# Kernel optimization log

Measured on AMD Instinct MI355X. Metric: run time of the kernel, lower is better.

Reference implementation:

```python
import jax, jax.numpy as jnp
import numpy as np

N_NODES = 100000
N_EDGES = 3200000
R0, R1, R2, N1 = 16, 8, 16, 32


def setup_inputs() -> dict:
    key = jax.random.key(0)
    ks = jax.random.split(key, 12)
    x = jax.random.normal(ks[0], (N_NODES, R0), dtype=jnp.float32)
    edge_index = jax.random.randint(ks[1], (2, N_EDGES), 0, N_NODES, dtype=jnp.int64)
    s = 0.1
    return {
        "x": x,
        "edge_index": edge_index,
        # GraphConv 1: lin_rel (weight+bias) applied to aggregated neighbors, lin_root (no bias) to self
        "W_rel1": jax.random.normal(ks[2], (R0, R1), dtype=jnp.float32) * s,
        "b_rel1": jnp.zeros((R1,), dtype=jnp.float32),
        "W_root1": jax.random.normal(ks[3], (R0, R1), dtype=jnp.float32) * s,
        # GraphConv 2
        "W_rel2": jax.random.normal(ks[4], (R1, R2), dtype=jnp.float32) * s,
        "b_rel2": jnp.zeros((R2,), dtype=jnp.float32),
        "W_root2": jax.random.normal(ks[5], (R1, R2), dtype=jnp.float32) * s,
        # fc layers
        "W_fc1": jax.random.normal(ks[6], (R2, N1), dtype=jnp.float32) * s,
        "b_fc1": jnp.zeros((N1,), dtype=jnp.float32),
        "W_fc2": jax.random.normal(ks[7], (N1, 1), dtype=jnp.float32) * s,
        "b_fc2": jnp.zeros((1,), dtype=jnp.float32),
    }


def _graph_conv(x, src, dst, W_rel, b_rel, W_root):
    # GraphConv with aggr='add': out_i = lin_rel(sum_{j->i} x_j) + lin_root(x_i)
    agg = jax.ops.segment_sum(x[src], dst, num_segments=N_NODES)  # [N, d_in]
    return agg @ W_rel + b_rel + x @ W_root


def reference(x, edge_index,
              W_rel1, b_rel1, W_root1,
              W_rel2, b_rel2, W_root2,
              W_fc1, b_fc1, W_fc2, b_fc2):
    src, dst = edge_index[0], edge_index[1]
    h = jax.nn.relu(_graph_conv(x, src, dst, W_rel1, b_rel1, W_root1))
    h = jax.nn.relu(_graph_conv(h, src, dst, W_rel2, b_rel2, W_root2))
    h = jax.nn.relu(h @ W_fc1 + b_fc1)
    out = h @ W_fc2 + b_fc2  # [N, 1]
    return out - jnp.mean(out)
```

## Files before the change

kernel.cpp:

```cpp
#include <hip/hip_runtime.h>

#define NN 100000
#define NE 3200000
#define BSH 7
#define BNODES 128
#define NBUCK 782
#define BCAP 4800
#define BIN_CHUNK 8192
#define NBIN_BLOCKS ((NE + BIN_CHUNK - 1) / BIN_CHUNK)

#define S1 2097152.0f
#define S2 524288.0f
#define INV_S1 (1.0f / S1)
#define INV_S2 (1.0f / S2)

__global__ void node_layer1(const float* __restrict__ x,
                            const float* __restrict__ Wrel1,
                            const float* __restrict__ brel1,
                            const float* __restrict__ Wroot1,
                            int* __restrict__ y1q,
                            int* __restrict__ initq,
                            int* __restrict__ bucketCnt ) {
    __shared__ float sW[16 * 8];
    __shared__ float sR[16 * 8];
    __shared__ float sb[8];
    int t = threadIdx.x;
    if (t < 128) { sW[t] = Wrel1[t]; sR[t] = Wroot1[t]; }
    if (t < 8)   { sb[t] = brel1[t]; }
    if (blockIdx.x == 0) {
        for (int k = t; k < NBUCK + 1; k += 256) bucketCnt[k] = 0;
    }
    __syncthreads();

    int i = blockIdx.x * blockDim.x + t;
    if (i >= NN) return;

    const float4* xp = (const float4*)(x + (size_t)i * 16);
    float4 x0 = xp[0], x1 = xp[1], x2 = xp[2], x3 = xp[3];
    float xi[16] = {x0.x, x0.y, x0.z, x0.w, x1.x, x1.y, x1.z, x1.w,
                    x2.x, x2.y, x2.z, x2.w, x3.x, x3.y, x3.z, x3.w};

    float y[8], r[8];
#pragma unroll
    for (int j = 0; j < 8; ++j) { y[j] = 0.0f; r[j] = sb[j]; }
#pragma unroll
    for (int k = 0; k < 16; ++k) {
        float xv = xi[k];
#pragma unroll
        for (int j = 0; j < 8; ++j) {
            y[j] = fmaf(xv, sW[k * 8 + j], y[j]);
            r[j] = fmaf(xv, sR[k * 8 + j], r[j]);
        }
    }
    int4* yp = (int4*)(y1q + (size_t)i * 8);
    int4* ap = (int4*)(initq + (size_t)i * 8);
    int4 q0, q1, p0, p1;
    q0.x = __float2int_rn(y[0] * S1); q0.y = __float2int_rn(y[1] * S1);
    q0.z = __float2int_rn(y[2] * S1); q0.w = __float2int_rn(y[3] * S1);
    q1.x = __float2int_rn(y[4] * S1); q1.y = __float2int_rn(y[5] * S1);
    q1.z = __float2int_rn(y[6] * S1); q1.w = __float2int_rn(y[7] * S1);
    p0.x = __float2int_rn(r[0] * S1); p0.y = __float2int_rn(r[1] * S1);
    p0.z = __float2int_rn(r[2] * S1); p0.w = __float2int_rn(r[3] * S1);
    p1.x = __float2int_rn(r[4] * S1); p1.y = __float2int_rn(r[5] * S1);
    p1.z = __float2int_rn(r[6] * S1); p1.w = __float2int_rn(r[7] * S1);
    yp[0] = q0; yp[1] = q1;
    ap[0] = p0; ap[1] = p1;
}

__global__ __launch_bounds__(1024) void binning(const int* __restrict__ src,
                                                const int* __restrict__ dst,
                                                int* __restrict__ bucketCnt,
                                                int* __restrict__ bpay) {
    __shared__ int stage[BIN_CHUNK];
    __shared__ int hist[NBUCK];
    __shared__ int loff[NBUCK + 1];
    __shared__ int gbase[NBUCK];
    __shared__ int psum[1024];

    int t = threadIdx.x;
    int e0 = blockIdx.x * BIN_CHUNK;
    int nE = NE - e0; if (nE > BIN_CHUNK) nE = BIN_CHUNK;
    int nv = nE >> 2;

    if (t < NBUCK) hist[t] = 0;
    __syncthreads();

    const int4* dst4 = (const int4*)(dst + e0);
    const int4* src4 = (const int4*)(src + e0);

    for (int k = t; k < nv; k += 1024) {
        int4 d4 = dst4[k];
        atomicAdd(&hist[d4.x >> BSH], 1);
        atomicAdd(&hist[d4.y >> BSH], 1);
        atomicAdd(&hist[d4.z >> BSH], 1);
        atomicAdd(&hist[d4.w >> BSH], 1);
    }
    __syncthreads();

    int c = (t < NBUCK) ? hist[t] : 0;
    psum[t] = c;
    __syncthreads();
    for (int off = 1; off < 1024; off <<= 1) {
        int u = (t >= off) ? psum[t - off] : 0;
        __syncthreads();
        psum[t] += u;
        __syncthreads();
    }
    if (t < NBUCK) loff[t] = psum[t] - c;
    if (t == 0) loff[NBUCK] = nE;
    __syncthreads();

    if (t < NBUCK) {
        gbase[t] = c ? atomicAdd(&bucketCnt[t], c) : 0;
        hist[t] = loff[t];
    }
    __syncthreads();

    for (int k = t; k < nv; k += 1024) {
        int4 d4 = dst4[k];
        int4 s4 = src4[k];
        int b, r;
        b = d4.x >> BSH; r = atomicAdd(&hist[b], 1);
        stage[r] = ((d4.x & (BNODES - 1)) << 17) | s4.x;
        b = d4.y >> BSH; r = atomicAdd(&hist[b], 1);
        stage[r] = ((d4.y & (BNODES - 1)) << 17) | s4.y;
        b = d4.z >> BSH; r = atomicAdd(&hist[b], 1);
        stage[r] = ((d4.z & (BNODES - 1)) << 17) | s4.z;
        b = d4.w >> BSH; r = atomicAdd(&hist[b], 1);
        stage[r] = ((d4.w & (BNODES - 1)) << 17) | s4.w;
    }
    __syncthreads();

    for (int p = t; p < nE; p += 1024) {
        int lo = 0, hi = NBUCK - 1;
        while (lo < hi) {
            int mid = (lo + hi + 1) >> 1;
            if (loff[mid] <= p) lo = mid; else hi = mid - 1;
        }
        int ob = gbase[lo] + (p - loff[lo]);
        if (ob < BCAP) bpay[lo * BCAP + ob] = stage[p];
    }
}

__global__ __launch_bounds__(512, 6) void bucket_agg1(const int* __restrict__ bucketCnt,
                                                      const int* __restrict__ bpay,
                                                      const int* __restrict__ y1q,
                                                      int* __restrict__ h1q ) {
    __shared__ int qacc[BNODES * 8];
    int t = threadIdx.x;
    int b = blockIdx.x;
    int gb = b * BCAP;
    int fbase = b * (BNODES * 8);

    for (int k = t; k < BNODES * 8; k += 512) {
        int gi = fbase + k;
        qacc[k] = (gi < NN * 8) ? h1q[gi] : 0;
    }
    int C = bucketCnt[b]; if (C > BCAP) C = BCAP;
    __syncthreads();

    int f = t & 7, g = t >> 3;
    const int4* bp4 = (const int4*)(bpay + gb);
    int iters = C >> 9;
    for (int it = 0; it < iters; ++it) {
        int4 va = bp4[(it << 7) + (g << 1)];
        int4 vb = bp4[(it << 7) + (g << 1) + 1];
        int a0 = y1q[((va.x & 0x1FFFF) << 3) + f];
        int a1 = y1q[((va.y & 0x1FFFF) << 3) + f];
        int a2 = y1q[((va.z & 0x1FFFF) << 3) + f];
        int a3 = y1q[((va.w & 0x1FFFF) << 3) + f];
        int a4 = y1q[((vb.x & 0x1FFFF) << 3) + f];
        int a5 = y1q[((vb.y & 0x1FFFF) << 3) + f];
        int a6 = y1q[((vb.z & 0x1FFFF) << 3) + f];
        int a7 = y1q[((vb.w & 0x1FFFF) << 3) + f];
        atomicAdd(&qacc[((va.x >> 17) << 3) + f], a0);
        atomicAdd(&qacc[((va.y >> 17) << 3) + f], a1);
        atomicAdd(&qacc[((va.z >> 17) << 3) + f], a2);
        atomicAdd(&qacc[((va.w >> 17) << 3) + f], a3);
        atomicAdd(&qacc[((vb.x >> 17) << 3) + f], a4);
        atomicAdd(&qacc[((vb.y >> 17) << 3) + f], a5);
        atomicAdd(&qacc[((vb.z >> 17) << 3) + f], a6);
        atomicAdd(&qacc[((vb.w >> 17) << 3) + f], a7);
    }
    for (int e = (iters << 9) + g; e < C; e += 64) {
        int v = bpay[gb + e];
        int a = y1q[((v & 0x1FFFF) << 3) + f];
        atomicAdd(&qacc[((v >> 17) << 3) + f], a);
    }
    __syncthreads();

    for (int k = t; k < BNODES * 8; k += 512) {
        int gi = fbase + k;
        if (gi < NN * 8) {
            float h = (float)qacc[k] * INV_S1;
            h = h > 0.0f ? h : 0.0f;
            h1q[gi] = __float2int_rn(h * S2);
        }
    }
}

__global__ __launch_bounds__(512, 6) void bucket_agg2_tail(const int* __restrict__ bucketCnt,
                                                           const int* __restrict__ bpay,
                                                           const int* __restrict__ h1q,
                                                           const float* __restrict__ Wrel2,
                                                           const float* __restrict__ brel2,
                                                           const float* __restrict__ Wroot2,
                                                           const float* __restrict__ Wfc1,
                                                           const float* __restrict__ bfc1,
                                                           const float* __restrict__ Wfc2,
                                                           const float* __restrict__ bfc2,
                                                           float* __restrict__ out,
                                                           float* __restrict__ gsum) {
    __shared__ int qacc[BNODES * 8];
    __shared__ float sWrel2[128], sWroot2[128], sbrel2[16];
    __shared__ float sWfc1[512], sbfc1[32], sWfc2[32];
    __shared__ float sbfc2;
    __shared__ float wsum[8];

    int t = threadIdx.x;
    int b = blockIdx.x;
    int gb = b * BCAP;
    int n0 = b * BNODES;

    for (int k = t; k < BNODES * 8; k += 512) qacc[k] = 0;
    sWfc1[t] = Wfc1[t];
    if (t < 128) { sWrel2[t] = Wrel2[t]; sWroot2[t] = Wroot2[t]; }
    if (t >= 128 && t < 144) sbrel2[t - 128] = brel2[t - 128];
    if (t >= 192 && t < 224) { sbfc1[t - 192] = bfc1[t - 192]; sWfc2[t - 192] = Wfc2[t - 192]; }
    if (t == 256) sbfc2 = bfc2[0];
    int C = bucketCnt[b]; if (C > BCAP) C = BCAP;
    __syncthreads();

    int f = t & 7, g = t >> 3;
    const int4* bp4 = (const int4*)(bpay + gb);
    int iters = C >> 9;
    for (int it = 0; it < iters; ++it) {
        int4 va = bp4[(it << 7) + (g << 1)];
        int4 vb = bp4[(it << 7) + (g << 1) + 1];
        int a0 = h1q[((va.x & 0x1FFFF) << 3) + f];
        int a1 = h1q[((va.y & 0x1FFFF) << 3) + f];
        int a2 = h1q[((va.z & 0x1FFFF) << 3) + f];
        int a3 = h1q[((va.w & 0x1FFFF) << 3) + f];
        int a4 = h1q[((vb.x & 0x1FFFF) << 3) + f];
        int a5 = h1q[((vb.y & 0x1FFFF) << 3) + f];
        int a6 = h1q[((vb.z & 0x1FFFF) << 3) + f];
        int a7 = h1q[((vb.w & 0x1FFFF) << 3) + f];
        atomicAdd(&qacc[((va.x >> 17) << 3) + f], a0);
        atomicAdd(&qacc[((va.y >> 17) << 3) + f], a1);
        atomicAdd(&qacc[((va.z >> 17) << 3) + f], a2);
        atomicAdd(&qacc[((va.w >> 17) << 3) + f], a3);
        atomicAdd(&qacc[((vb.x >> 17) << 3) + f], a4);
        atomicAdd(&qacc[((vb.y >> 17) << 3) + f], a5);
        atomicAdd(&qacc[((vb.z >> 17) << 3) + f], a6);
        atomicAdd(&qacc[((vb.w >> 17) << 3) + f], a7);
    }
    for (int e = (iters << 9) + g; e < C; e += 64) {
        int v = bpay[gb + e];
        int a = h1q[((v & 0x1FFFF) << 3) + f];
        atomicAdd(&qacc[((v >> 17) << 3) + f], a);
    }
    __syncthreads();

    float o = 0.0f;
    int node = n0 + t;
    if (t < BNODES && node < NN) {
        const int4* hp = (const int4*)(h1q + (size_t)node * 8);
        int4 ha = hp[0], hb = hp[1];
        float h1v[8] = {ha.x * INV_S2, ha.y * INV_S2, ha.z * INV_S2, ha.w * INV_S2,
                        hb.x * INV_S2, hb.y * INV_S2, hb.z * INV_S2, hb.w * INV_S2};
        float s2[8];
#pragma unroll
        for (int j = 0; j < 8; ++j) s2[j] = (float)qacc[t * 8 + j] * INV_S2;

        float h2[16];
#pragma unroll
        for (int j = 0; j < 16; ++j) h2[j] = sbrel2[j];
#pragma unroll
        for (int k = 0; k < 8; ++k) {
            float sv = s2[k], hv = h1v[k];
#pragma unroll
            for (int j = 0; j < 16; ++j) {
                h2[j] = fmaf(sv, sWrel2[k * 16 + j], h2[j]);
                h2[j] = fmaf(hv, sWroot2[k * 16 + j], h2[j]);
            }
        }
#pragma unroll
        for (int j = 0; j < 16; ++j) h2[j] = h2[j] > 0.0f ? h2[j] : 0.0f;

        o = sbfc2;
#pragma unroll
        for (int m = 0; m < 32; ++m) {
            float a = sbfc1[m];
#pragma unroll
            for (int j = 0; j < 16; ++j) a = fmaf(h2[j], sWfc1[j * 32 + m], a);
            a = a > 0.0f ? a : 0.0f;
            o = fmaf(a, sWfc2[m], o);
        }
        out[node] = o;
    }

    float v = o;
#pragma unroll
    for (int off = 32; off > 0; off >>= 1) v += __shfl_down(v, off);
    int lane = t & 63, w = t >> 6;
    if (lane == 0) wsum[w] = v;
    __syncthreads();
    if (t == 0) {
        float s = 0.0f;
#pragma unroll
        for (int k = 0; k < 8; ++k) s += wsum[k];
        atomicAdd(gsum, s);
    }
}

__global__ void subtract_mean(float* __restrict__ out,
                              const float* __restrict__ gsum) {
    int i = blockIdx.x * blockDim.x + threadIdx.x;
    if (i < NN) out[i] -= (*gsum) * (1.0f / (float)NN);
}

extern "C" void kernel_launch(void* const* d_in, const int* in_sizes, int n_in,
                              void* d_out, int out_size, void* d_ws, size_t ws_size,
                              hipStream_t stream) {
    const float* x      = (const float*)d_in[0];
    const int*   ei     = (const int*)d_in[1];
    const float* Wrel1  = (const float*)d_in[2];
    const float* brel1  = (const float*)d_in[3];
    const float* Wroot1 = (const float*)d_in[4];
    const float* Wrel2  = (const float*)d_in[5];
    const float* brel2  = (const float*)d_in[6];
    const float* Wroot2 = (const float*)d_in[7];
    const float* Wfc1   = (const float*)d_in[8];
    const float* bfc1   = (const float*)d_in[9];
    const float* Wfc2   = (const float*)d_in[10];
    const float* bfc2   = (const float*)d_in[11];
    float* out = (float*)d_out;
    float* ws  = (float*)d_ws;

    int*   y1q       = (int*)ws;
    int*   h1q       = (int*)(ws + 800000);
    int*   bucketCnt = (int*)(ws + 1600000);
    float* gsum      = ws + 1600782;
    int*   bpay      = (int*)(ws + 1600783);

    const int* src = ei;
    const int* dst = ei + NE;

    node_layer1<<<(NN + 255) / 256, 256, 0, stream>>>(x, Wrel1, brel1, Wroot1,
                                                      y1q, h1q, bucketCnt);
    binning<<<NBIN_BLOCKS, 1024, 0, stream>>>(src, dst, bucketCnt, bpay);
    bucket_agg1<<<NBUCK, 512, 0, stream>>>(bucketCnt, bpay, y1q, h1q);
    bucket_agg2_tail<<<NBUCK, 512, 0, stream>>>(bucketCnt, bpay, h1q,
                                                Wrel2, brel2, Wroot2,
                                                Wfc1, bfc1, Wfc2, bfc2, out, gsum);
    subtract_mean<<<(NN + 255) / 256, 256, 0, stream>>>(out, gsum);
}
```

Before: 183.1 us.

## Fuse layer-1 node transform into binning kernel and streamline bucket scatter

Merges the node_layer1 kernel into the binning kernel as extra blocks, and zeroes bucket counters with a memset instead of inside a kernel. The binning path keeps each thread's edges in registers instead of reloading them, replaces the shared-memory block scan with wave shuffle scans, and stores each edge's global destination next to its payload so the final scatter needs no binary search. It also raises the occupancy hint on bucket_agg1. The aim is to cut launches, syncs and per-edge search work, at the cost of more shared memory per binning block (int2 staging).

```diff
diff --git a/kernel.cpp b/kernel.cpp
--- a/kernel.cpp
+++ b/kernel.cpp
@@ -8,76 +8,75 @@
 #define BCAP 4800
 #define BIN_CHUNK 8192
 #define NBIN_BLOCKS ((NE + BIN_CHUNK - 1) / BIN_CHUNK)
+#define NL1_BLOCKS ((NN + 1023) / 1024)
 
 #define S1 2097152.0f
 #define S2 524288.0f
 #define INV_S1 (1.0f / S1)
 #define INV_S2 (1.0f / S2)
 
-__global__ void node_layer1(const float* __restrict__ x,
-                            const float* __restrict__ Wrel1,
-                            const float* __restrict__ brel1,
-                            const float* __restrict__ Wroot1,
-                            int* __restrict__ y1q,
-                            int* __restrict__ initq,
-                            int* __restrict__ bucketCnt ) {
-    __shared__ float sW[16 * 8];
-    __shared__ float sR[16 * 8];
-    __shared__ float sb[8];
+__global__ __launch_bounds__(1024, 8) void bin_and_l1(
+        const float* __restrict__ x,
+        const float* __restrict__ Wrel1,
+        const float* __restrict__ brel1,
+        const float* __restrict__ Wroot1,
+        const int* __restrict__ src,
+        const int* __restrict__ dst,
+        int* __restrict__ y1q,
+        int* __restrict__ initq,
+        int* __restrict__ bucketCnt,
+        int* __restrict__ bpay) {
     int t = threadIdx.x;
-    if (t < 128) { sW[t] = Wrel1[t]; sR[t] = Wroot1[t]; }
-    if (t < 8)   { sb[t] = brel1[t]; }
-    if (blockIdx.x == 0) {
-        for (int k = t; k < NBUCK + 1; k += 256) bucketCnt[k] = 0;
-    }
-    __syncthreads();
-
-    int i = blockIdx.x * blockDim.x + t;
-    if (i >= NN) return;
-
-    const float4* xp = (const float4*)(x + (size_t)i * 16);
-    float4 x0 = xp[0], x1 = xp[1], x2 = xp[2], x3 = xp[3];
-    float xi[16] = {x0.x, x0.y, x0.z, x0.w, x1.x, x1.y, x1.z, x1.w,
-                    x2.x, x2.y, x2.z, x2.w, x3.x, x3.y, x3.z, x3.w};
-
-    float y[8], r[8];
-#pragma unroll
-    for (int j = 0; j < 8; ++j) { y[j] = 0.0f; r[j] = sb[j]; }
-#pragma unroll
-    for (int k = 0; k < 16; ++k) {
-        float xv = xi[k];
-#pragma unroll
-        for (int j = 0; j < 8; ++j) {
-            y[j] = fmaf(xv, sW[k * 8 + j], y[j]);
-            r[j] = fmaf(xv, sR[k * 8 + j], r[j]);
-        }
-    }
-    int4* yp = (int4*)(y1q + (size_t)i * 8);
-    int4* ap = (int4*)(initq + (size_t)i * 8);
-    int4 q0, q1, p0, p1;
-    q0.x = __float2int_rn(y[0] * S1); q0.y = __float2int_rn(y[1] * S1);
-    q0.z = __float2int_rn(y[2] * S1); q0.w = __float2int_rn(y[3] * S1);
-    q1.x = __float2int_rn(y[4] * S1); q1.y = __float2int_rn(y[5] * S1);
-    q1.z = __float2int_rn(y[6] * S1); q1.w = __float2int_rn(y[7] * S1);
-    p0.x = __float2int_rn(r[0] * S1); p0.y = __float2int_rn(r[1] * S1);
-    p0.z = __float2int_rn(r[2] * S1); p0.w = __float2int_rn(r[3] * S1);
-    p1.x = __float2int_rn(r[4] * S1); p1.y = __float2int_rn(r[5] * S1);
-    p1.z = __float2int_rn(r[6] * S1); p1.w = __float2int_rn(r[7] * S1);
-    yp[0] = q0; yp[1] = q1;
-    ap[0] = p0; ap[1] = p1;
-}
-
-__global__ __launch_bounds__(1024) void binning(const int* __restrict__ src,
-                                                const int* __restrict__ dst,
-                                                int* __restrict__ bucketCnt,
-                                                int* __restrict__ bpay) {
-    __shared__ int stage[BIN_CHUNK];
-    __shared__ int hist[NBUCK];
-    __shared__ int loff[NBUCK + 1];
-    __shared__ int gbase[NBUCK];
-    __shared__ int psum[1024];
-
-    int t = threadIdx.x;
+
+    if (blockIdx.x >= NBIN_BLOCKS) {
+        __shared__ float sW[16 * 8];
+        __shared__ float sR[16 * 8];
+        __shared__ float sb[8];
+        if (t < 128) { sW[t] = Wrel1[t]; sR[t] = Wroot1[t]; }
+        if (t < 8)   { sb[t] = brel1[t]; }
+        __syncthreads();
+
+        int i = (blockIdx.x - NBIN_BLOCKS) * 1024 + t;
+        if (i >= NN) return;
+
+        const float4* xp = (const float4*)(x + (size_t)i * 16);
+        float4 x0 = xp[0], x1 = xp[1], x2 = xp[2], x3 = xp[3];
+        float xi[16] = {x0.x, x0.y, x0.z, x0.w, x1.x, x1.y, x1.z, x1.w,
+                        x2.x, x2.y, x2.z, x2.w, x3.x, x3.y, x3.z, x3.w};
+
+        float y[8], r[8];
+#pragma unroll
+        for (int j = 0; j < 8; ++j) { y[j] = 0.0f; r[j] = sb[j]; }
+#pragma unroll
+        for (int k = 0; k < 16; ++k) {
+            float xv = xi[k];
+#pragma unroll
+            for (int j = 0; j < 8; ++j) {
+                y[j] = fmaf(xv, sW[k * 8 + j], y[j]);
+                r[j] = fmaf(xv, sR[k * 8 + j], r[j]);
+            }
+        }
+        int4* yp = (int4*)(y1q + (size_t)i * 8);
+        int4* ap = (int4*)(initq + (size_t)i * 8);
+        int4 q0, q1, p0, p1;
+        q0.x = __float2int_rn(y[0] * S1); q0.y = __float2int_rn(y[1] * S1);
+        q0.z = __float2int_rn(y[2] * S1); q0.w = __float2int_rn(y[3] * S1);
+        q1.x = __float2int_rn(y[4] * S1); q1.y = __float2int_rn(y[5] * S1);
+        q1.z = __float2int_rn(y[6] * S1); q1.w = __float2int_rn(y[7] * S1);
+        p0.x = __float2int_rn(r[0] * S1); p0.y = __float2int_rn(r[1] * S1);
+        p0.z = __float2int_rn(r[2] * S1); p0.w = __float2int_rn(r[3] * S1);
+        p1.x = __float2int_rn(r[4] * S1); p1.y = __float2int_rn(r[5] * S1);
+        p1.z = __float2int_rn(r[6] * S1); p1.w = __float2int_rn(r[7] * S1);
+        yp[0] = q0; yp[1] = q1;
+        ap[0] = p0; ap[1] = p1;
+        return;
+    }
+
+    __shared__ int2 stage2[BIN_CHUNK];
+    __shared__ int  hist[NBUCK];
+    __shared__ int  gdelta[NBUCK];
+    __shared__ int  wsum16[16];
+
     int e0 = blockIdx.x * BIN_CHUNK;
     int nE = NE - e0; if (nE > BIN_CHUNK) nE = BIN_CHUNK;
     int nv = nE >> 2;
@@ -88,61 +87,77 @@
     const int4* dst4 = (const int4*)(dst + e0);
     const int4* src4 = (const int4*)(src + e0);
 
-    for (int k = t; k < nv; k += 1024) {
-        int4 d4 = dst4[k];
-        atomicAdd(&hist[d4.x >> BSH], 1);
-        atomicAdd(&hist[d4.y >> BSH], 1);
-        atomicAdd(&hist[d4.z >> BSH], 1);
-        atomicAdd(&hist[d4.w >> BSH], 1);
+    int4 d0_, s0_, d1_, s1_;
+    bool h0 = (t < nv), h1 = (t + 1024 < nv);
+    if (h0) {
+        d0_ = dst4[t]; s0_ = src4[t];
+        atomicAdd(&hist[d0_.x >> BSH], 1);
+        atomicAdd(&hist[d0_.y >> BSH], 1);
+        atomicAdd(&hist[d0_.z >> BSH], 1);
+        atomicAdd(&hist[d0_.w >> BSH], 1);
+    }
+    if (h1) {
+        d1_ = dst4[t + 1024]; s1_ = src4[t + 1024];
+        atomicAdd(&hist[d1_.x >> BSH], 1);
+        atomicAdd(&hist[d1_.y >> BSH], 1);
+        atomicAdd(&hist[d1_.z >> BSH], 1);
+        atomicAdd(&hist[d1_.w >> BSH], 1);
     }
     __syncthreads();
 
     int c = (t < NBUCK) ? hist[t] : 0;
-    psum[t] = c;
-    __syncthreads();
-    for (int off = 1; off < 1024; off <<= 1) {
-        int u = (t >= off) ? psum[t - off] : 0;
-        __syncthreads();
-        psum[t] += u;
-        __syncthreads();
-    }
-    if (t < NBUCK) loff[t] = psum[t] - c;
-    if (t == 0) loff[NBUCK] = nE;
-    __syncthreads();
+    int lane = t & 63, w = t >> 6;
+    int pref = c;
+#pragma unroll
+    for (int off = 1; off < 64; off <<= 1) {
+        int u = __shfl_up(pref, off);
+        if (lane >= off) pref += u;
+    }
+    if (lane == 63) wsum16[w] = pref;
+    __syncthreads();
+    if (t < 16) {
+        int s = wsum16[t];
+#pragma unroll
+        for (int off = 1; off < 16; off <<= 1) {
+            int u = __shfl_up(s, off);
+            if (t >= off) s += u;
+        }
+        wsum16[t] = s;
+    }
+    __syncthreads();
+    int base = w ? wsum16[w - 1] : 0;
+    int excl = base + pref - c;
 
     if (t < NBUCK) {
-        gbase[t] = c ? atomicAdd(&bucketCnt[t], c) : 0;
-        hist[t] = loff[t];
-    }
-    __syncthreads();
-
-    for (int k = t; k < nv; k += 1024) {
-        int4 d4 = dst4[k];
-        int4 s4 = src4[k];
-        int b, r;
-        b = d4.x >> BSH; r = atomicAdd(&hist[b], 1);
-        stage[r] = ((d4.x & (BNODES - 1)) << 17) | s4.x;
-        b = d4.y >> BSH; r = atomicAdd(&hist[b], 1);
-        stage[r] = ((d4.y & (BNODES - 1)) << 17) | s4.y;
-        b = d4.z >> BSH; r = atomicAdd(&hist[b], 1);
-        stage[r] = ((d4.z & (BNODES - 1)) << 17) | s4.z;
-        b = d4.w >> BSH; r = atomicAdd(&hist[b], 1);
-        stage[r] = ((d4.w & (BNODES - 1)) << 17) | s4.w;
-    }
+        int gb0 = c ? atomicAdd(&bucketCnt[t], c) : 0;
+        hist[t] = excl;
+        gdelta[t] = t * BCAP + gb0 - excl;
+    }
+    __syncthreads();
+
+#define PLACE1(dv, sv) do {                                              \
+        int b_ = (dv) >> BSH;                                            \
+        int r_ = atomicAdd(&hist[b_], 1);                                \
+        int ga_ = r_ + gdelta[b_];                                       \
+        int2 e_; e_.x = (((dv) & (BNODES - 1)) << 17) | (sv);            \
+        e_.y = (ga_ < (b_ + 1) * BCAP) ? ga_ : -1;                       \
+        stage2[r_] = e_;                                                 \
+    } while (0)
+
+    if (h0) { PLACE1(d0_.x, s0_.x); PLACE1(d0_.y, s0_.y);
+              PLACE1(d0_.z, s0_.z); PLACE1(d0_.w, s0_.w); }
+    if (h1) { PLACE1(d1_.x, s1_.x); PLACE1(d1_.y, s1_.y);
+              PLACE1(d1_.z, s1_.z); PLACE1(d1_.w, s1_.w); }
+#undef PLACE1
     __syncthreads();
 
     for (int p = t; p < nE; p += 1024) {
-        int lo = 0, hi = NBUCK - 1;
-        while (lo < hi) {
-            int mid = (lo + hi + 1) >> 1;
-            if (loff[mid] <= p) lo = mid; else hi = mid - 1;
-        }
-        int ob = gbase[lo] + (p - loff[lo]);
-        if (ob < BCAP) bpay[lo * BCAP + ob] = stage[p];
-    }
-}
-
-__global__ __launch_bounds__(512, 6) void bucket_agg1(const int* __restrict__ bucketCnt,
+        int2 e = stage2[p];
+        if (e.y >= 0) bpay[e.y] = e.x;
+    }
+}
+
+__global__ __launch_bounds__(512, 8) void bucket_agg1(const int* __restrict__ bucketCnt,
                                                       const int* __restrict__ bpay,
                                                       const int* __restrict__ y1q,
                                                       int* __restrict__ h1q ) {
@@ -346,9 +361,10 @@
     const int* src = ei;
     const int* dst = ei + NE;
 
-    node_layer1<<<(NN + 255) / 256, 256, 0, stream>>>(x, Wrel1, brel1, Wroot1,
-                                                      y1q, h1q, bucketCnt);
-    binning<<<NBIN_BLOCKS, 1024, 0, stream>>>(src, dst, bucketCnt, bpay);
+    hipMemsetAsync(bucketCnt, 0, (NBUCK + 1) * sizeof(int), stream);
+    bin_and_l1<<<NBIN_BLOCKS + NL1_BLOCKS, 1024, 0, stream>>>(x, Wrel1, brel1, Wroot1,
+                                                              src, dst, y1q, h1q,
+                                                              bucketCnt, bpay);
     bucket_agg1<<<NBUCK, 512, 0, stream>>>(bucketCnt, bpay, y1q, h1q);
     bucket_agg2_tail<<<NBUCK, 512, 0, stream>>>(bucketCnt, bpay, h1q,
                                                 Wrel2, brel2, Wroot2,
```

Result: faster. 171.9 us (-6.1%).
